# Optimization experiments

Hardware: AMD Instinct MI355X
Metric: run time of the kernel (lower is better)

The kernel has to match this reference:

```python
import jax, jax.numpy as jnp
import numpy as np

GRID_SIZE = 4
SPLINE_ORDER = 3
EDGE_DIM = 384


def make_grid():
    # efficient-KAN default grid_range [-1, 1]
    h = 2.0 / GRID_SIZE
    return (jnp.arange(-SPLINE_ORDER, GRID_SIZE + SPLINE_ORDER + 1, dtype=jnp.float32) * h - 1.0)


def b_splines(x, grid, k):
    # x: (N, d); grid: (G+2k+1,) shared across features -> (N, d, G+k)
    xe = x[..., None]
    bases = ((xe >= grid[:-1]) & (xe < grid[1:])).astype(x.dtype)
    for j in range(1, k + 1):
        bases = ((xe - grid[: -(j + 1)]) / (grid[j:-1] - grid[: -(j + 1)]) * bases[..., :-1]
                 + (grid[j + 1:] - xe) / (grid[j + 1:] - grid[1:-j]) * bases[..., 1:])
    return bases


def kan_linear(x, base_W, spline_W, grid):
    # efficient-KAN KANLinear: silu base path + spline path
    base = jax.nn.silu(x) @ base_W.T
    B = b_splines(x, grid, SPLINE_ORDER)          # (N, in, G+k)
    spline = jnp.einsum('nic,oic->no', B, spline_W)
    return base + spline


def gckan_layer(x, edge_index, edge_attr, p, grid):
    ea = edge_attr @ p['edge_W'].T + p['edge_b']          # (E, out)
    xt = x @ p['node_W'].T + p['node_b']                  # (N, out)
    row, col = edge_index[0], edge_index[1]
    msg = ea * xt[row]                                    # gather + multiply
    agg = jnp.zeros_like(xt).at[col].add(msg)             # scatter-add
    return kan_linear(agg, p['base_W'], p['spline_W'], grid)


def _layer_params(key, in_feat, out_feat):
    k1, k2, k3, k4 = jax.random.split(key, 4)
    coef = GRID_SIZE + SPLINE_ORDER
    return {
        'node_W': jax.random.normal(k1, (out_feat, in_feat), jnp.float32) / np.sqrt(in_feat),
        'node_b': jnp.zeros((out_feat,), jnp.float32),
        'edge_W': jax.random.normal(k2, (out_feat, EDGE_DIM), jnp.float32) / np.sqrt(EDGE_DIM),
        'edge_b': jnp.zeros((out_feat,), jnp.float32),
        'base_W': jax.random.normal(k3, (out_feat, out_feat), jnp.float32) / np.sqrt(out_feat),
        'spline_W': jax.random.normal(k4, (out_feat, out_feat, coef), jnp.float32) * (0.1 / np.sqrt(out_feat)),
    }


def setup_inputs() -> dict:
    N, E, F, H, C = 50000, 500000, 256, 256, 32
    key = jax.random.key(0)
    ks = jax.random.split(key, 6)
    inp = {
        'x': jax.random.normal(ks[0], (N, F), jnp.float32),
        'edge_index': jax.random.randint(ks[1], (2, E), 0, N, jnp.int32),
        'edge_attr': jax.random.normal(ks[2], (E, EDGE_DIM), jnp.float32),
    }
    p0 = _layer_params(ks[3], F, H)
    p1 = _layer_params(ks[4], H, H)
    po = _layer_params(ks[5], F + 2 * H, C)
    for tag, p in (('0', p0), ('1', p1), ('o', po)):
        for n, v in p.items():
            inp[n + tag] = v
    return inp


def reference(x, edge_index, edge_attr,
              node_W0, node_b0, edge_W0, edge_b0, base_W0, spline_W0,
              node_W1, node_b1, edge_W1, edge_b1, base_W1, spline_W1,
              node_Wo, node_bo, edge_Wo, edge_bo, base_Wo, spline_Wo):
    grid = make_grid()
    p0 = dict(node_W=node_W0, node_b=node_b0, edge_W=edge_W0, edge_b=edge_b0, base_W=base_W0, spline_W=spline_W0)
    p1 = dict(node_W=node_W1, node_b=node_b1, edge_W=edge_W1, edge_b=edge_b1, base_W=base_W1, spline_W=spline_W1)
    po = dict(node_W=node_Wo, node_b=node_bo, edge_W=edge_Wo, edge_b=edge_bo, base_W=base_Wo, spline_W=spline_Wo)
    skips = [x]
    h = gckan_layer(x, edge_index, edge_attr, p0, grid)
    skips.append(h)
    h = gckan_layer(h, edge_index, edge_attr, p1, grid)
    skips.append(h)
    h = jnp.concatenate(skips, axis=1)  # skip=True concat -> (N, F+2H)
    return gckan_layer(h, edge_index, edge_attr, po, grid)
```

## Files before the change

### kernel.cpp

```cpp
#include <hip/hip_runtime.h>


typedef __attribute__((ext_vector_type(4))) float f32x4;
typedef __attribute__((ext_vector_type(8))) short bf16x8;
typedef __attribute__((ext_vector_type(8))) unsigned short u16x8;
typedef __attribute__((ext_vector_type(4))) unsigned short u16x4;

__device__ __forceinline__ unsigned short f2bf(float f) {
    union { float f; unsigned u; } v; v.f = f;
    unsigned r = v.u + 0x7FFFu + ((v.u >> 16) & 1u);
    return (unsigned short)(r >> 16);
}

__device__ __forceinline__ float bf2f(unsigned short u) {
    union { unsigned u; float f; } v; v.u = ((unsigned)u) << 16;
    return v.f;
}

__device__ __forceinline__ float siluf(float x) {
    return x / (1.0f + __expf(-x));
}

__device__ __forceinline__ void gl16(const void* g, void* l) {
    __builtin_amdgcn_global_load_lds(
        (const __attribute__((address_space(1))) unsigned*)g,
        (__attribute__((address_space(3))) unsigned*)l, 16, 0, 0);
}

__device__ __forceinline__ void expand8(float x, float* o8) {
    float b[10];
#pragma unroll
    for (int i = 0; i < 10; ++i) {
        float ti = 0.5f * i - 2.5f;
        b[i] = (x >= ti && x < ti + 0.5f) ? 1.0f : 0.0f;
    }
#pragma unroll
    for (int j = 1; j <= 3; ++j) {
        float inv = 2.0f / (float)j;
#pragma unroll
        for (int i = 0; i < 10 - j; ++i) {
            float ti = 0.5f * i - 2.5f;
            float tj = 0.5f * (i + j + 1) - 2.5f;
            b[i] = (x - ti) * inv * b[i] + (tj - x) * inv * b[i + 1];
        }
    }
    o8[0] = siluf(x);
#pragma unroll
    for (int c = 0; c < 7; ++c) o8[c + 1] = b[c];
}

__global__ __launch_bounds__(256) void k_hist(
    const int* __restrict__ col, int* __restrict__ cnt, int E) {
    int i = blockIdx.x * 256 + threadIdx.x;
    if (i < E) atomicAdd(&cnt[col[i]], 1);
}

__global__ __launch_bounds__(1024) void k_scan(int* __restrict__ c, int N) {
    __shared__ int wsum[16];
    __shared__ int ctot;
    const int t = threadIdx.x;
    const int lane = t & 63, wid = t >> 6;
    int carry = 0;
    for (int base = 0; base < N; base += 1024) {
        int i = base + t;
        int v0 = (i < N) ? c[i] : 0;
        int v = v0;
#pragma unroll
        for (int off = 1; off < 64; off <<= 1) {
            int n = __shfl_up(v, (unsigned)off, 64);
            if (lane >= off) v += n;
        }
        if (lane == 63) wsum[wid] = v;
        __syncthreads();
        if (t < 16) {
            int s = wsum[t], sv = s;
#pragma unroll
            for (int off = 1; off < 16; off <<= 1) {
                int n = __shfl_up(sv, (unsigned)off, 16);
                if (t >= off) sv += n;
            }
            wsum[t] = sv - s;
            if (t == 15) ctot = sv;
        }
        __syncthreads();
        if (i < N) c[i] = carry + wsum[wid] + v - v0;
        carry += ctot;
        __syncthreads();
    }
}

__global__ __launch_bounds__(256) void k_scatter(
    const int* __restrict__ row, const int* __restrict__ col,
    int* __restrict__ cursor, int* __restrict__ rowS,
    int* __restrict__ colS, int* __restrict__ eidS, int E) {
    int i = blockIdx.x * 256 + threadIdx.x;
    if (i < E) {
        int c = col[i];
        int p = atomicAdd(&cursor[c], 1);
        rowS[p] = row[i];
        colS[p] = c;
        eidS[p] = i;
    }
}

__global__ __launch_bounds__(256) void pack_kt(
    const float* __restrict__ src, unsigned short* __restrict__ dst,
    int N, int K) {
    long idx = (long)blockIdx.x * 256 + threadIdx.x;
    if (idx >= (long)N * K) return;
    int n = (int)(idx / K), k = (int)(idx - (long)n * K);
    long o = (((long)(k >> 5) * 4 + ((k >> 3) & 3)) * N + n) * 8 + (k & 7);
    dst[o] = f2bf(src[idx]);
}

__global__ __launch_bounds__(256) void pack_kan_kt(
    const float* __restrict__ baseW, const float* __restrict__ splineW,
    unsigned short* __restrict__ dst, int N) {
    long idx = (long)blockIdx.x * 256 + threadIdx.x;
    if (idx >= (long)N * 2048) return;
    int n = (int)(idx >> 11), k = (int)(idx & 2047);
    int ic = k >> 3, c = k & 7;
    float v = (c == 0) ? baseW[(long)n * 256 + ic]
                       : splineW[((long)n * 256 + ic) * 7 + (c - 1)];
    long o = (((long)(k >> 5) * 4 + ((k >> 3) & 3)) * N + n) * 8 + (k & 7);
    dst[o] = f2bf(v);
}

template <bool TWO, bool WITH_O>
__global__ __launch_bounds__(256, 1) void ea_gemm6(
    const float* __restrict__ EA,
    const unsigned short* __restrict__ Wp0, const float* __restrict__ b0,
    const unsigned short* __restrict__ Wp1, const float* __restrict__ b1,
    const unsigned short* __restrict__ Wpo, const float* __restrict__ bo,
    unsigned short* __restrict__ O0, unsigned short* __restrict__ O1,
    unsigned short* __restrict__ Oo, int E) {
    constexpr int BSZ = TWO ? 32768 : 16384;
    constexpr int WOOFF = 8192 + 3 * BSZ;
    constexpr int SMEMSZ = WOOFF + (WITH_O ? 24576 : 0);
    __shared__ __align__(16) char smem[SMEMSZ];

    const int tid = threadIdx.x;
    const int wv = tid >> 6, lane = tid & 63;
    const int l15 = lane & 15, l4 = lane >> 4;
    const long m0 = (long)blockIdx.x * 64;

    f32x4 acc0[4][4] = {};
    f32x4 acc1[4][4] = {};
    f32x4 acco[4] = {};

    const int sr = tid >> 2, sg = tid & 3;
    const long arow = m0 + sr;
    const bool aok = arow < E;
    const float* aptr = EA + arow * 384 + sg * 8;
    const int awoff = sg * 1024 + ((sr ^ (sg << 2))) * 16;

    const char* wp0 = (const char*)Wp0;
    const char* wp1 = (const char*)Wp1;
    const int ci = lane * 16;

    if (WITH_O) {
#pragma unroll
        for (int i = 0; i < 6; ++i) {
            int o = (tid + i * 256) * 16;
            *(u16x8*)(smem + WOOFF + o) = *(const u16x8*)((const char*)Wpo + o);
        }
    }

#define ISSUE_B6(IT, BUF)                                                      \
    {                                                                          \
        _Pragma("unroll")                                                      \
        for (int g = 0; g < 4; ++g) {                                          \
            int ch = g * 4 + wv;                                               \
            gl16(wp0 + (long)(IT) * 16384 + ch * 1024 + ci,                    \
                 smem + 8192 + (BUF) * BSZ + ch * 1024);                       \
        }                                                                      \
        if (TWO) {                                                             \
            _Pragma("unroll")                                                  \
            for (int g = 0; g < 4; ++g) {                                      \
                int ch = g * 4 + wv;                                           \
                gl16(wp1 + (long)(IT) * 16384 + ch * 1024 + ci,                \
                     smem + 8192 + (BUF) * BSZ + 16384 + ch * 1024);           \
            }                                                                  \
        }                                                                      \
        __builtin_amdgcn_sched_barrier(0);                                     \
    }

#define WRITE_A6(IT, VA, VB)                                                   \
    {                                                                          \
        u16x8 rr = {};                                                         \
        if (aok) {                                                             \
            rr[0] = f2bf((VA).x); rr[1] = f2bf((VA).y);                        \
            rr[2] = f2bf((VA).z); rr[3] = f2bf((VA).w);                        \
            rr[4] = f2bf((VB).x); rr[5] = f2bf((VB).y);                        \
            rr[6] = f2bf((VB).z); rr[7] = f2bf((VB).w);                        \
        }                                                                      \
        *(u16x8*)(smem + ((IT) & 1) * 4096 + awoff) = rr;                      \
        __builtin_amdgcn_sched_barrier(0);                                     \
    }

    const float4 z4 = make_float4(0.f, 0.f, 0.f, 0.f);
    {
        float4 s0 = z4, s1 = z4;
        if (aok) { s0 = *(const float4*)(aptr); s1 = *(const float4*)(aptr + 4); }
        WRITE_A6(0, s0, s1);
    }
    float4 r1a = z4, r1b = z4, r0a = z4, r0b = z4;
    if (aok) { r1a = *(const float4*)(aptr + 32); r1b = *(const float4*)(aptr + 36); }
    __builtin_amdgcn_sched_barrier(0);
    ISSUE_B6(0, 0);
    if (aok) { r0a = *(const float4*)(aptr + 64); r0b = *(const float4*)(aptr + 68); }
    __builtin_amdgcn_sched_barrier(0);
    ISSUE_B6(1, 1);

#pragma unroll
    for (int it = 0; it < 12; ++it) {
        if (it <= 9) {
            if (TWO) asm volatile("s_waitcnt vmcnt(10)" ::: "memory");
            else     asm volatile("s_waitcnt vmcnt(6)"  ::: "memory");
        } else if (it == 10) {
            if (TWO) asm volatile("s_waitcnt vmcnt(8)" ::: "memory");
            else     asm volatile("s_waitcnt vmcnt(4)" ::: "memory");
        } else {
            asm volatile("s_waitcnt vmcnt(0)" ::: "memory");
        }
        asm volatile("s_waitcnt lgkmcnt(0)" ::: "memory");
        __builtin_amdgcn_s_barrier();
        __builtin_amdgcn_sched_barrier(0);

        if (it < 11) {
            if ((it + 1) & 1) { WRITE_A6(it + 1, r1a, r1b); }
            else              { WRITE_A6(it + 1, r0a, r0b); }
        }
        if (it <= 8) {
            if ((it + 3) & 1) {
                if (aok) {
                    r1a = *(const float4*)(aptr + (it + 3) * 32);
                    r1b = *(const float4*)(aptr + (it + 3) * 32 + 4);
                }
            } else {
                if (aok) {
                    r0a = *(const float4*)(aptr + (it + 3) * 32);
                    r0b = *(const float4*)(aptr + (it + 3) * 32 + 4);
                }
            }
            __builtin_amdgcn_sched_barrier(0);
        }
        if (it <= 9) { ISSUE_B6(it + 2, (it + 2) % 3); }

        const int abuf = it & 1, bbuf = it % 3;
        bf16x8 af[4];
#pragma unroll
        for (int mi = 0; mi < 4; ++mi)
            af[mi] = *(const bf16x8*)(smem + abuf * 4096 + l4 * 1024 +
                                      (((mi * 16 + l15) ^ (l4 << 2))) * 16);
        {
            bf16x8 bf0[4];
#pragma unroll
            for (int nj = 0; nj < 4; ++nj)
                bf0[nj] = *(const bf16x8*)(smem + 8192 + bbuf * BSZ + l4 * 4096 +
                                           (wv * 64 + nj * 16 + l15) * 16);
#pragma unroll
            for (int mi = 0; mi < 4; ++mi)
#pragma unroll
                for (int nj = 0; nj < 4; ++nj)
                    acc0[mi][nj] = __builtin_amdgcn_mfma_f32_16x16x32_bf16(
                        af[mi], bf0[nj], acc0[mi][nj], 0, 0, 0);
        }
        if (TWO) {
            bf16x8 bf1[4];
#pragma unroll
            for (int nj = 0; nj < 4; ++nj)
                bf1[nj] = *(const bf16x8*)(smem + 8192 + bbuf * BSZ + 16384 +
                                           l4 * 4096 + (wv * 64 + nj * 16 + l15) * 16);
#pragma unroll
            for (int mi = 0; mi < 4; ++mi)
#pragma unroll
                for (int nj = 0; nj < 4; ++nj)
                    acc1[mi][nj] = __builtin_amdgcn_mfma_f32_16x16x32_bf16(
                        af[mi], bf1[nj], acc1[mi][nj], 0, 0, 0);
        }
        if (WITH_O && wv < 2) {
            bf16x8 bov = *(const bf16x8*)(smem + WOOFF + it * 2048 + l4 * 512 +
                                          (wv * 16 + l15) * 16);
#pragma unroll
            for (int mi = 0; mi < 4; ++mi)
                acco[mi] = __builtin_amdgcn_mfma_f32_16x16x32_bf16(
                    af[mi], bov, acco[mi], 0, 0, 0);
        }
    }
#undef ISSUE_B6
#undef WRITE_A6

    const int nb2 = wv * 64;
    float bs0[4];
#pragma unroll
    for (int nj = 0; nj < 4; ++nj) bs0[nj] = b0[nb2 + nj * 16 + l15];
#pragma unroll
    for (int mi = 0; mi < 4; ++mi) {
#pragma unroll
        for (int r = 0; r < 4; ++r) {
            long e = m0 + mi * 16 + l4 * 4 + r;
            if (e < E) {
                unsigned short* dst = O0 + e * 256 + nb2 + l15;
#pragma unroll
                for (int nj = 0; nj < 4; ++nj)
                    dst[nj * 16] = f2bf(acc0[mi][nj][r] + bs0[nj]);
            }
        }
    }
    if (TWO) {
        float bs1[4];
#pragma unroll
        for (int nj = 0; nj < 4; ++nj) bs1[nj] = b1[nb2 + nj * 16 + l15];
#pragma unroll
        for (int mi = 0; mi < 4; ++mi) {
#pragma unroll
            for (int r = 0; r < 4; ++r) {
                long e = m0 + mi * 16 + l4 * 4 + r;
                if (e < E) {
                    unsigned short* dst = O1 + e * 256 + nb2 + l15;
#pragma unroll
                    for (int nj = 0; nj < 4; ++nj)
                        dst[nj * 16] = f2bf(acc1[mi][nj][r] + bs1[nj]);
                }
            }
        }
    }
    if (WITH_O && wv < 2) {
        float bso = bo[wv * 16 + l15];
#pragma unroll
        for (int mi = 0; mi < 4; ++mi) {
#pragma unroll
            for (int r = 0; r < 4; ++r) {
                long e = m0 + mi * 16 + l4 * 4 + r;
                if (e < E)
                    Oo[e * 32 + wv * 16 + l15] = f2bf(acco[mi][r] + bso);
            }
        }
    }
}

__global__ __launch_bounds__(256) void kan_mfma256_p(
    const float* __restrict__ AGG, const unsigned short* __restrict__ Wp,
    float* __restrict__ Y, int M) {
    __shared__ __align__(16) char smem[8192 + 2 * 16384];
    const int tid = threadIdx.x;
    const int wv = tid >> 6, lane = tid & 63;
    const int l15 = lane & 15, l4 = lane >> 4;
    const long m0 = (long)blockIdx.x * 64;
    f32x4 acc[4][4] = {};

    const int srow = tid & 63, sg = tid >> 6;
    const long arow = m0 + srow;
    const bool aok = arow < M;
    const float* aptr = AGG + arow * 256 + sg;
    const char* wp = (const char*)Wp;
    const int ci = lane * 16;
    const int awoff = sg * 1024 + srow * 16;

#define ISSUE_KB(IT, BUF)                                                      \
    {                                                                          \
        _Pragma("unroll")                                                      \
        for (int g = 0; g < 4; ++g) {                                          \
            int ch = g * 4 + wv;                                               \
            gl16(wp + (long)(IT) * 16384 + ch * 1024 + ci,                     \
                 smem + 8192 + (BUF) * 16384 + ch * 1024);                     \
        }                                                                      \
        __builtin_amdgcn_sched_barrier(0);                                     \
    }

    float xv0 = aok ? aptr[0] : 0.f;
    ISSUE_KB(0, 0);
    {
        float e8[8];
        expand8(xv0, e8);
        u16x8 ap;
#pragma unroll
        for (int c = 0; c < 8; ++c) ap[c] = f2bf(e8[c]);
        *(u16x8*)(smem + awoff) = ap;
    }
    float xv1 = aok ? aptr[4] : 0.f;
    __builtin_amdgcn_sched_barrier(0);

    for (int it = 0; it < 64; ++it) {
        if (it == 63) asm volatile("s_waitcnt vmcnt(0)" ::: "memory");
        else          asm volatile("s_waitcnt vmcnt(1)" ::: "memory");
        asm volatile("s_waitcnt lgkmcnt(0)" ::: "memory");
        __builtin_amdgcn_s_barrier();
        __builtin_amdgcn_sched_barrier(0);
        const int buf = it & 1, nbf = buf ^ 1;
        if (it < 63) {
            ISSUE_KB(it + 1, nbf);
            {
                float e8[8];
                expand8(xv1, e8);
                u16x8 ap;
#pragma unroll
                for (int c = 0; c < 8; ++c) ap[c] = f2bf(e8[c]);
                *(u16x8*)(smem + nbf * 4096 + awoff) = ap;
            }
            __builtin_amdgcn_sched_barrier(0);
            if (it < 62) {
                xv1 = aok ? aptr[(it + 2) * 4] : 0.f;
                __builtin_amdgcn_sched_barrier(0);
            }
        }
        bf16x8 af[4], bfv[4];
#pragma unroll
        for (int mi = 0; mi < 4; ++mi)
            af[mi] = *(const bf16x8*)(smem + buf * 4096 + l4 * 1024 +
                                      (mi * 16 + l15) * 16);
#pragma unroll
        for (int nj = 0; nj < 4; ++nj)
            bfv[nj] = *(const bf16x8*)(smem + 8192 + buf * 16384 + l4 * 4096 +
                                       (wv * 64 + nj * 16 + l15) * 16);
#pragma unroll
        for (int mi = 0; mi < 4; ++mi)
#pragma unroll
            for (int nj = 0; nj < 4; ++nj)
                acc[mi][nj] = __builtin_amdgcn_mfma_f32_16x16x32_bf16(
                    af[mi], bfv[nj], acc[mi][nj], 0, 0, 0);
    }
#undef ISSUE_KB

    const int nb = wv * 64;
#pragma unroll
    for (int mi = 0; mi < 4; ++mi) {
#pragma unroll
        for (int r = 0; r < 4; ++r) {
            long gm = m0 + mi * 16 + l4 * 4 + r;
            if (gm < M) {
#pragma unroll
                for (int nj = 0; nj < 4; ++nj)
                    Y[gm * 256 + nb + nj * 16 + l15] = acc[mi][nj][r];
            }
        }
    }
}

template <int K>
__global__ __launch_bounds__(256) void node_mfma_p(
    const float* __restrict__ X, const unsigned short* __restrict__ Wp,
    const float* __restrict__ bias, unsigned short* __restrict__ Y, int M) {
    __shared__ __align__(16) char smem[8192 + 2 * 16384];
    const int tid = threadIdx.x;
    const int wv = tid >> 6, lane = tid & 63;
    const int l15 = lane & 15, l4 = lane >> 4;
    const long m0 = (long)blockIdx.x * 64;
    f32x4 acc[4][4] = {};
    constexpr int NIT = K / 32;

    const int sr = tid >> 2, sg = tid & 3;
    const long arow = m0 + sr;
    const bool aok = arow < M;
    const float* aptr = X + arow * K + sg * 8;
    const int awoff = sg * 1024 + ((sr ^ (sg << 2))) * 16;
    const char* wp = (const char*)Wp;
    const int ci = lane * 16;

#define ISSUE_NB(IT, BUF)                                                      \
    {                                                                          \
        _Pragma("unroll")                                                      \
        for (int g = 0; g < 4; ++g) {                                          \
            int ch = g * 4 + wv;                                               \
            gl16(wp + (long)(IT) * 16384 + ch * 1024 + ci,                     \
                 smem + 8192 + (BUF) * 16384 + ch * 1024);                     \
        }                                                                      \
        __builtin_amdgcn_sched_barrier(0);                                     \
    }

#define WRITE_NA(BUF)                                                          \
    {                                                                          \
        u16x8 rr = {};                                                         \
        if (aok) {                                                             \
            rr[0] = f2bf(a0v.x); rr[1] = f2bf(a0v.y);                          \
            rr[2] = f2bf(a0v.z); rr[3] = f2bf(a0v.w);                          \
            rr[4] = f2bf(a1v.x); rr[5] = f2bf(a1v.y);                          \
            rr[6] = f2bf(a1v.z); rr[7] = f2bf(a1v.w);                          \
        }                                                                      \
        *(u16x8*)(smem + (BUF) * 4096 + awoff) = rr;                           \
        __builtin_amdgcn_sched_barrier(0);                                     \
    }

    ISSUE_NB(0, 0);
    float4 a0v = make_float4(0.f, 0.f, 0.f, 0.f);
    float4 a1v = make_float4(0.f, 0.f, 0.f, 0.f);
    if (aok) { a0v = *(const float4*)(aptr); a1v = *(const float4*)(aptr + 4); }
    WRITE_NA(0);
    if (aok) { a0v = *(const float4*)(aptr + 32); a1v = *(const float4*)(aptr + 36); }
    __builtin_amdgcn_sched_barrier(0);

#pragma unroll
    for (int it = 0; it < NIT; ++it) {
        if (it == NIT - 1) asm volatile("s_waitcnt vmcnt(0)" ::: "memory");
        else               asm volatile("s_waitcnt vmcnt(2)" ::: "memory");
        asm volatile("s_waitcnt lgkmcnt(0)" ::: "memory");
        __builtin_amdgcn_s_barrier();
        __builtin_amdgcn_sched_barrier(0);
        const int buf = it & 1, nbf = buf ^ 1;
        if (it < NIT - 1) {
            ISSUE_NB(it + 1, nbf);
            WRITE_NA(nbf);
            if (it < NIT - 2) {
                if (aok) {
                    a0v = *(const float4*)(aptr + (it + 2) * 32);
                    a1v = *(const float4*)(aptr + (it + 2) * 32 + 4);
                }
                __builtin_amdgcn_sched_barrier(0);
            }
        }
        bf16x8 af[4], bfv[4];
#pragma unroll
        for (int mi = 0; mi < 4; ++mi)
            af[mi] = *(const bf16x8*)(smem + buf * 4096 + l4 * 1024 +
                                      (((mi * 16 + l15) ^ (l4 << 2))) * 16);
#pragma unroll
        for (int nj = 0; nj < 4; ++nj)
            bfv[nj] = *(const bf16x8*)(smem + 8192 + buf * 16384 + l4 * 4096 +
                                       (wv * 64 + nj * 16 + l15) * 16);
#pragma unroll
        for (int mi = 0; mi < 4; ++mi)
#pragma unroll
            for (int nj = 0; nj < 4; ++nj)
                acc[mi][nj] = __builtin_amdgcn_mfma_f32_16x16x32_bf16(
                    af[mi], bfv[nj], acc[mi][nj], 0, 0, 0);
    }
#undef ISSUE_NB
#undef WRITE_NA

    const int nb = wv * 64;
    float bs[4];
#pragma unroll
    for (int nj = 0; nj < 4; ++nj) bs[nj] = bias[nb + nj * 16 + l15];
#pragma unroll
    for (int mi = 0; mi < 4; ++mi) {
#pragma unroll
        for (int r = 0; r < 4; ++r) {
            long gm = m0 + mi * 16 + l4 * 4 + r;
            if (gm < M) {
#pragma unroll
                for (int nj = 0; nj < 4; ++nj)
                    Y[gm * 256 + nb + nj * 16 + l15] = f2bf(acc[mi][nj][r] + bs[nj]);
            }
        }
    }
}

__global__ __launch_bounds__(256) void msg256(
    const unsigned short* __restrict__ EAr, const unsigned short* __restrict__ XT,
    const int* __restrict__ rowS, const int* __restrict__ colS,
    const int* __restrict__ eidS, float* __restrict__ AGG, int E) {
    __shared__ __align__(16) unsigned short eas[64][264];
    __shared__ int rows_s[64];
    __shared__ int cols_s[64];
    const int tid = threadIdx.x;
    const long m0 = (long)blockIdx.x * 64;

    const int r = tid >> 2, s = tid & 3;
    {
        long p = m0 + r;
        if (p < E) {
            const unsigned short* src = EAr + (long)eidS[p] * 256 + s * 8;
#pragma unroll
            for (int k = 0; k < 8; ++k)
                *(u16x8*)&eas[r][s * 8 + k * 32] = *(const u16x8*)(src + k * 32);
        } else {
            u16x8 z = {};
#pragma unroll
            for (int k = 0; k < 8; ++k) *(u16x8*)&eas[r][s * 8 + k * 32] = z;
        }
    }
    if (tid < 64) {
        long p = m0 + tid;
        cols_s[tid] = (p < E) ? colS[p] : -1;
        rows_s[tid] = (p < E) ? rowS[p] : 0;
    }
    __syncthreads();

    const int c = tid;
    float sum = 0.f;
    int cur = cols_s[0];
    int runstart = 0;
#pragma unroll 1
    for (int g = 0; g < 8; ++g) {
        float xv[8];
#pragma unroll
        for (int j = 0; j < 8; ++j)
            xv[j] = bf2f(XT[(long)rows_s[g * 8 + j] * 256 + c]);
#pragma unroll
        for (int j = 0; j < 8; ++j) {
            int e = g * 8 + j;
            int cc = cols_s[e];
            if (cc != cur) {
                if (cur >= 0) {
                    float* dst = AGG + (long)cur * 256 + c;
                    if (runstart > 0) *dst = sum;
                    else atomicAdd(dst, sum);
                }
                cur = cc; runstart = e; sum = 0.f;
            }
            sum += bf2f(eas[e][c]) * xv[j];
        }
    }
    if (cur >= 0) {
        atomicAdd(AGG + (long)cur * 256 + c, sum);
    }
}

__global__ __launch_bounds__(256) void msg32(
    const unsigned short* __restrict__ EAro, const unsigned short* __restrict__ XT,
    const int* __restrict__ rowS, const int* __restrict__ colS,
    const int* __restrict__ eidS, float* __restrict__ AGG, int E) {
    __shared__ __align__(16) unsigned short eas[256][36];
    __shared__ int rows_s[256];
    __shared__ int cols_s[256];
    __shared__ int eid_s[256];
    const int tid = threadIdx.x;
    const long m0 = (long)blockIdx.x * 256;

    {
        long p = m0 + tid;
        cols_s[tid] = (p < E) ? colS[p] : -1;
        rows_s[tid] = (p < E) ? rowS[p] : 0;
        eid_s[tid]  = (p < E) ? eidS[p] : -1;
    }
    __syncthreads();
    const int rr0 = tid >> 2, s = tid & 3;
#pragma unroll
    for (int ps = 0; ps < 4; ++ps) {
        int rr = ps * 64 + rr0;
        int eid = eid_s[rr];
        u16x8 v = {};
        if (eid >= 0) v = *(const u16x8*)(EAro + (long)eid * 32 + s * 8);
        *(u16x8*)&eas[rr][s * 8] = v;
    }
    __syncthreads();

    const int c = tid & 31, sb = tid >> 5;
    const int e0 = sb * 32;
    float sum = 0.f;
    int cur = cols_s[e0];
    int runstart = e0;
#pragma unroll 1
    for (int g = 0; g < 4; ++g) {
        float xv[8];
#pragma unroll
        for (int j = 0; j < 8; ++j)
            xv[j] = bf2f(XT[(long)rows_s[e0 + g * 8 + j] * 32 + c]);
#pragma unroll
        for (int j = 0; j < 8; ++j) {
            int e = e0 + g * 8 + j;
            int cc = cols_s[e];
            if (cc != cur) {
                if (cur >= 0) {
                    float* dst = AGG + (long)cur * 32 + c;
                    if (runstart > 0 && cols_s[runstart - 1] != cur) *dst = sum;
                    else atomicAdd(dst, sum);
                }
                cur = cc; runstart = e; sum = 0.f;
            }
            sum += bf2f(eas[e][c]) * xv[j];
        }
    }
    if (cur >= 0) {
        int eend = e0 + 32;
        float* dst = AGG + (long)cur * 32 + c;
        bool oks = (runstart > 0 && cols_s[runstart - 1] != cur);
        bool oke = (eend < 256 && cols_s[eend] != cur);
        if (oks && oke) *dst = sum;
        else atomicAdd(dst, sum);
    }
}

__global__ __launch_bounds__(256) void node_cat_mfma(
    const float* __restrict__ X, const float* __restrict__ H0,
    const float* __restrict__ H1, const unsigned short* __restrict__ Wh,
    const float* __restrict__ bias, unsigned short* __restrict__ Y, int M) {
    __shared__ __align__(16) unsigned short As[4][256][8];
    __shared__ __align__(16) unsigned short Bs[4][32][8];
    const int tid = threadIdx.x;
    const int wv = tid >> 6, lane = tid & 63;
    const int l15 = lane & 15, l4 = lane >> 4;
    const long m0 = (long)blockIdx.x * 256;
    f32x4 acc[4][2] = {};

    const int sr = tid >> 3;
    const int sq = (tid & 7) * 4;
    const int sg2 = sq >> 3, so2 = sq & 7;

    for (int it = 0; it < 24; ++it) {
        const int k0 = it * 32;
        const float* src = (it < 8) ? X : (it < 16) ? H0 : H1;
        const int kk = k0 & 255;
        float4 va[8];
#pragma unroll
        for (int j = 0; j < 8; ++j) {
            long r_ = m0 + j * 32 + sr;
            va[j] = (r_ < M) ? *(const float4*)(src + r_ * 256 + kk + sq)
                             : make_float4(0.f, 0.f, 0.f, 0.f);
        }
        u16x8 bv = {};
        if (tid < 128)
            bv = *(const u16x8*)(Wh + (long)(tid >> 2) * 768 + k0 + (tid & 3) * 8);
        __syncthreads();
#pragma unroll
        for (int j = 0; j < 8; ++j) {
            u16x4 ap;
            ap[0] = f2bf(va[j].x); ap[1] = f2bf(va[j].y);
            ap[2] = f2bf(va[j].z); ap[3] = f2bf(va[j].w);
            *(u16x4*)&As[sg2][j * 32 + sr][so2] = ap;
        }
        if (tid < 128) *(u16x8*)&Bs[tid & 3][tid >> 2][0] = bv;
        __syncthreads();
        bf16x8 af[4], bfv[2];
#pragma unroll
        for (int mi = 0; mi < 4; ++mi)
            af[mi] = *(const bf16x8*)&As[l4][wv * 64 + mi * 16 + l15][0];
#pragma unroll
        for (int nj = 0; nj < 2; ++nj)
            bfv[nj] = *(const bf16x8*)&Bs[l4][nj * 16 + l15][0];
#pragma unroll
        for (int mi = 0; mi < 4; ++mi)
#pragma unroll
            for (int nj = 0; nj < 2; ++nj)
                acc[mi][nj] = __builtin_amdgcn_mfma_f32_16x16x32_bf16(
                    af[mi], bfv[nj], acc[mi][nj], 0, 0, 0);
    }

#pragma unroll
    for (int mi = 0; mi < 4; ++mi) {
#pragma unroll
        for (int r = 0; r < 4; ++r) {
            long gm = m0 + wv * 64 + mi * 16 + l4 * 4 + r;
            if (gm < M) {
#pragma unroll
                for (int nj = 0; nj < 2; ++nj) {
                    int o = nj * 16 + l15;
                    Y[gm * 32 + o] = f2bf(acc[mi][nj][r] + bias[o]);
                }
            }
        }
    }
}

__global__ __launch_bounds__(256) void kan_gemm32(
    const float* __restrict__ AGG, const float* __restrict__ Wc,
    float* __restrict__ Y, int M) {
    __shared__ float As[64][36];
    __shared__ float Bs[32][36];
    const int tid = threadIdx.x;
    const int tx = tid & 15, ty = tid >> 4;
    const int m0 = blockIdx.x * 64;
    float acc[4][2] = {{0.f, 0.f}, {0.f, 0.f}, {0.f, 0.f}, {0.f, 0.f}};
    const int er = tid >> 2, ef = tid & 3;
    const int em = m0 + er;
    for (int ic = 0; ic < 32; ic += 4) {
        float xv = (em < M) ? AGG[(long)em * 32 + ic + ef] : 0.f;
        float e8[8];
        expand8(xv, e8);
        *(float4*)&As[er][ef * 8] = make_float4(e8[0], e8[1], e8[2], e8[3]);
        *(float4*)&As[er][ef * 8 + 4] = make_float4(e8[4], e8[5], e8[6], e8[7]);
        {
            int o = tid >> 3, k4 = (tid & 7) * 4;
            *(float4*)&Bs[o][k4] = *(const float4*)&Wc[(long)o * 256 + ic * 8 + k4];
        }
        __syncthreads();
#pragma unroll
        for (int kk = 0; kk < 32; ++kk) {
            float a_[4], b_[2];
#pragma unroll
            for (int i = 0; i < 4; ++i) a_[i] = As[ty * 4 + i][kk];
#pragma unroll
            for (int j = 0; j < 2; ++j) b_[j] = Bs[tx * 2 + j][kk];
#pragma unroll
            for (int i = 0; i < 4; ++i)
#pragma unroll
                for (int j = 0; j < 2; ++j) acc[i][j] = fmaf(a_[i], b_[j], acc[i][j]);
        }
        __syncthreads();
    }
#pragma unroll
    for (int i = 0; i < 4; ++i) {
        int gm = m0 + ty * 4 + i;
        if (gm >= M) continue;
#pragma unroll
        for (int j = 0; j < 2; ++j) Y[(long)gm * 32 + tx * 2 + j] = acc[i][j];
    }
}

__global__ __launch_bounds__(256) void cvt_bf16(
    const float* __restrict__ s, unsigned short* __restrict__ d, int n) {
    int i = blockIdx.x * 256 + threadIdx.x;
    if (i < n) d[i] = f2bf(s[i]);
}

__global__ __launch_bounds__(256) void pack_kan_f32(
    const float* __restrict__ baseW, const float* __restrict__ splineW,
    float* __restrict__ Wc, int n) {
    int idx = blockIdx.x * 256 + threadIdx.x;
    if (idx >= n) return;
    float* dst = Wc + (long)idx * 8;
    dst[0] = baseW[idx];
    const float* sw = splineW + (long)idx * 7;
#pragma unroll
    for (int c = 0; c < 7; ++c) dst[1 + c] = sw[c];
}

extern "C" void kernel_launch(void* const* d_in, const int* in_sizes, int n_in,
                              void* d_out, int out_size, void* d_ws, size_t ws_size,
                              hipStream_t stream) {
    const float* x          = (const float*)d_in[0];
    const int*   edge_index = (const int*)d_in[1];
    const float* edge_attr  = (const float*)d_in[2];
    const float* node_W0 = (const float*)d_in[3];
    const float* node_b0 = (const float*)d_in[4];
    const float* edge_W0 = (const float*)d_in[5];
    const float* edge_b0 = (const float*)d_in[6];
    const float* base_W0 = (const float*)d_in[7];
    const float* spline_W0 = (const float*)d_in[8];
    const float* node_W1 = (const float*)d_in[9];
    const float* node_b1 = (const float*)d_in[10];
    const float* edge_W1 = (const float*)d_in[11];
    const float* edge_b1 = (const float*)d_in[12];
    const float* base_W1 = (const float*)d_in[13];
    const float* spline_W1 = (const float*)d_in[14];
    const float* node_Wo = (const float*)d_in[15];
    const float* node_bo = (const float*)d_in[16];
    const float* edge_Wo = (const float*)d_in[17];
    const float* edge_bo = (const float*)d_in[18];
    const float* base_Wo = (const float*)d_in[19];
    const float* spline_Wo = (const float*)d_in[20];
    float* out = (float*)d_out;

    const int N = in_sizes[0] / 256;
    const int E = in_sizes[1] / 2;

    float* ws  = (float*)d_ws;
    unsigned short* xt = (unsigned short*)ws;
    float* agg = ws + (long)N * 256;
    float* h0  = agg + (long)N * 256;
    float* h1  = h0 + (long)N * 256;
    float* Wco = h1 + (long)N * 256;
    unsigned short* Wp0  = (unsigned short*)(Wco + 32 * 256);
    unsigned short* Wp1  = Wp0 + 98304;
    unsigned short* Wpo  = Wp1 + 98304;
    unsigned short* nWp0 = Wpo + 12288;
    unsigned short* nWp1 = nWp0 + 65536;
    unsigned short* Wc0p = nWp1 + 65536;
    unsigned short* Wc1p = Wc0p + 524288;
    unsigned short* nWoh = Wc1p + 524288;
    int* cursor = (int*)(nWoh + 24576);
    int* rowS   = cursor + (N + 1);
    int* colS   = rowS + E;
    int* eidS   = colS + E;
    unsigned short* EAr0 = (unsigned short*)(((uintptr_t)(eidS + E) + 255) & ~(uintptr_t)255);
    const int nt256 = (E + 255) / 256;
    const long Epad = (long)nt256 * 256;
    unsigned short* EAr1 = EAr0 + Epad * 256;

    const size_t need2 = (size_t)((char*)(EAr1 + Epad * 256 + Epad * 32) - (char*)d_ws);
    const bool two = ws_size >= need2;
    unsigned short* EAro = two ? (EAr1 + Epad * 256) : (EAr0 + Epad * 256);

    const int* row = edge_index;
    const int* col = edge_index + E;

    const int nb64 = (N + 63) / 64;
    const int eb64 = (E + 63) / 64;
    const int eb256 = (E + 255) / 256;
    const int nb256 = (N + 255) / 256;

    hipMemsetAsync(cursor, 0, (size_t)(N + 1) * sizeof(int), stream);
    k_hist<<<eb256, 256, 0, stream>>>(col, cursor, E);
    k_scan<<<1, 1024, 0, stream>>>(cursor, N);
    k_scatter<<<eb256, 256, 0, stream>>>(row, col, cursor, rowS, colS, eidS, E);

    pack_kt<<<(256 * 384 + 255) / 256, 256, 0, stream>>>(edge_W0, Wp0, 256, 384);
    pack_kt<<<(256 * 384 + 255) / 256, 256, 0, stream>>>(edge_W1, Wp1, 256, 384);
    pack_kt<<<(32 * 384 + 255) / 256, 256, 0, stream>>>(edge_Wo, Wpo, 32, 384);
    pack_kt<<<(256 * 256 + 255) / 256, 256, 0, stream>>>(node_W0, nWp0, 256, 256);
    pack_kt<<<(256 * 256 + 255) / 256, 256, 0, stream>>>(node_W1, nWp1, 256, 256);
    pack_kan_kt<<<(256 * 2048 + 255) / 256, 256, 0, stream>>>(base_W0, spline_W0, Wc0p, 256);
    pack_kan_kt<<<(256 * 2048 + 255) / 256, 256, 0, stream>>>(base_W1, spline_W1, Wc1p, 256);
    cvt_bf16<<<(32 * 768 + 255) / 256, 256, 0, stream>>>(node_Wo, nWoh, 32 * 768);
    pack_kan_f32<<<(32 * 32 + 255) / 256, 256, 0, stream>>>(base_Wo, spline_Wo, Wco, 32 * 32);

    if (two) {
        ea_gemm6<true, true><<<eb64, 256, 0, stream>>>(
            edge_attr, Wp0, edge_b0, Wp1, edge_b1, Wpo, edge_bo,
            EAr0, EAr1, EAro, E);
    } else {
        ea_gemm6<false, true><<<eb64, 256, 0, stream>>>(
            edge_attr, Wp0, edge_b0, Wp0, edge_b0, Wpo, edge_bo,
            EAr0, EAr0, EAro, E);
    }

    hipMemsetAsync(agg, 0, (size_t)N * 256 * sizeof(float), stream);
    node_mfma_p<256><<<nb64, 256, 0, stream>>>(x, nWp0, node_b0, xt, N);
    msg256<<<eb64, 256, 0, stream>>>(EAr0, xt, rowS, colS, eidS, agg, E);
    kan_mfma256_p<<<nb64, 256, 0, stream>>>(agg, Wc0p, h0, N);

    if (!two) {
        ea_gemm6<false, false><<<eb64, 256, 0, stream>>>(
            edge_attr, Wp1, edge_b1, Wp1, edge_b1, Wpo, edge_bo,
            EAr0, EAr0, EAro, E);
    }
    hipMemsetAsync(agg, 0, (size_t)N * 256 * sizeof(float), stream);
    node_mfma_p<256><<<nb64, 256, 0, stream>>>(h0, nWp1, node_b1, xt, N);
    msg256<<<eb64, 256, 0, stream>>>(two ? EAr1 : EAr0, xt, rowS, colS, eidS, agg, E);
    kan_mfma256_p<<<nb64, 256, 0, stream>>>(agg, Wc1p, h1, N);

    hipMemsetAsync(agg, 0, (size_t)N * 32 * sizeof(float), stream);
    node_cat_mfma<<<nb256, 256, 0, stream>>>(x, h0, h1, nWoh, node_bo, xt, N);
    msg32<<<eb256, 256, 0, stream>>>(EAro, xt, rowS, colS, eidS, agg, E);
    kan_gemm32<<<nb64, 256, 0, stream>>>(agg, Wco, out, N);
}
```

Baseline: 1.459 ms.

## Double-buffer edge GEMM weights and stream Wo tiles to fit two blocks per CU

The edge-attribute GEMM kernel goes from a triple-buffered B pipeline with a fully preloaded Wo slice to a double-buffered pipeline. The Wo weights now stream per K-step through global_load_lds, issued by the two waves that do not run the Wo MFMAs. The smaller LDS footprint plus launch_bounds(256,2) is meant to let two blocks share a CU and hide memory latency across blocks. In exchange, prefetch depth drops to one stage and the tighter vmcnt waits may stall more within a block, and the register cap may cause spills given the two 4x4 accumulator arrays.

```diff
diff --git a/kernel.cpp b/kernel.cpp
--- a/kernel.cpp
+++ b/kernel.cpp
@@ -127,7 +127,7 @@
 }
 
 template <bool TWO, bool WITH_O>
-__global__ __launch_bounds__(256, 1) void ea_gemm6(
+__global__ __launch_bounds__(256, 2) void ea_gemm7(
     const float* __restrict__ EA,
     const unsigned short* __restrict__ Wp0, const float* __restrict__ b0,
     const unsigned short* __restrict__ Wp1, const float* __restrict__ b1,
@@ -135,8 +135,8 @@
     unsigned short* __restrict__ O0, unsigned short* __restrict__ O1,
     unsigned short* __restrict__ Oo, int E) {
     constexpr int BSZ = TWO ? 32768 : 16384;
-    constexpr int WOOFF = 8192 + 3 * BSZ;
-    constexpr int SMEMSZ = WOOFF + (WITH_O ? 24576 : 0);
+    constexpr int WOOFF = 8192 + 2 * BSZ;
+    constexpr int SMEMSZ = WOOFF + (WITH_O ? 4096 : 0);
     __shared__ __align__(16) char smem[SMEMSZ];
 
     const int tid = threadIdx.x;
@@ -156,17 +156,10 @@
 
     const char* wp0 = (const char*)Wp0;
     const char* wp1 = (const char*)Wp1;
+    const char* wpo = (const char*)Wpo;
     const int ci = lane * 16;
 
-    if (WITH_O) {
-#pragma unroll
-        for (int i = 0; i < 6; ++i) {
-            int o = (tid + i * 256) * 16;
-            *(u16x8*)(smem + WOOFF + o) = *(const u16x8*)((const char*)Wpo + o);
-        }
-    }
-
-#define ISSUE_B6(IT, BUF)                                                      \
+#define ISSUE_B7(IT, BUF)                                                      \
     {                                                                          \
         _Pragma("unroll")                                                      \
         for (int g = 0; g < 4; ++g) {                                          \
@@ -185,7 +178,15 @@
         __builtin_amdgcn_sched_barrier(0);                                     \
     }
 
-#define WRITE_A6(IT, VA, VB)                                                   \
+#define ISSUE_WO7(IT, BUF)                                                     \
+    {                                                                          \
+        if (WITH_O && wv >= 2)                                                 \
+            gl16(wpo + (long)(IT) * 2048 + (wv - 2) * 1024 + ci,               \
+                 smem + WOOFF + (BUF) * 2048 + (wv - 2) * 1024);               \
+        __builtin_amdgcn_sched_barrier(0);                                     \
+    }
+
+#define WRITE_A7(IT, VA, VB)                                                   \
     {                                                                          \
         u16x8 rr = {};                                                         \
         if (aok) {                                                             \
@@ -202,62 +203,57 @@
     {
         float4 s0 = z4, s1 = z4;
         if (aok) { s0 = *(const float4*)(aptr); s1 = *(const float4*)(aptr + 4); }
-        WRITE_A6(0, s0, s1);
+        WRITE_A7(0, s0, s1);
     }
     float4 r1a = z4, r1b = z4, r0a = z4, r0b = z4;
     if (aok) { r1a = *(const float4*)(aptr + 32); r1b = *(const float4*)(aptr + 36); }
     __builtin_amdgcn_sched_barrier(0);
-    ISSUE_B6(0, 0);
+    ISSUE_B7(0, 0);
+    ISSUE_WO7(0, 0);
     if (aok) { r0a = *(const float4*)(aptr + 64); r0b = *(const float4*)(aptr + 68); }
     __builtin_amdgcn_sched_barrier(0);
-    ISSUE_B6(1, 1);
 
 #pragma unroll
     for (int it = 0; it < 12; ++it) {
-        if (it <= 9) {
-            if (TWO) asm volatile("s_waitcnt vmcnt(10)" ::: "memory");
-            else     asm volatile("s_waitcnt vmcnt(6)"  ::: "memory");
-        } else if (it == 10) {
-            if (TWO) asm volatile("s_waitcnt vmcnt(8)" ::: "memory");
-            else     asm volatile("s_waitcnt vmcnt(4)" ::: "memory");
-        } else {
-            asm volatile("s_waitcnt vmcnt(0)" ::: "memory");
-        }
+        if (it <= 9) asm volatile("s_waitcnt vmcnt(2)" ::: "memory");
+        else         asm volatile("s_waitcnt vmcnt(0)" ::: "memory");
         asm volatile("s_waitcnt lgkmcnt(0)" ::: "memory");
         __builtin_amdgcn_s_barrier();
         __builtin_amdgcn_sched_barrier(0);
 
         if (it < 11) {
-            if ((it + 1) & 1) { WRITE_A6(it + 1, r1a, r1b); }
-            else              { WRITE_A6(it + 1, r0a, r0b); }
-        }
-        if (it <= 8) {
-            if ((it + 3) & 1) {
-                if (aok) {
-                    r1a = *(const float4*)(aptr + (it + 3) * 32);
-                    r1b = *(const float4*)(aptr + (it + 3) * 32 + 4);
+            const int nbf = (it + 1) & 1;
+            ISSUE_B7(it + 1, nbf);
+            ISSUE_WO7(it + 1, nbf);
+            if ((it + 1) & 1) { WRITE_A7(it + 1, r1a, r1b); }
+            else              { WRITE_A7(it + 1, r0a, r0b); }
+            if (it <= 8) {
+                if ((it + 3) & 1) {
+                    if (aok) {
+                        r1a = *(const float4*)(aptr + (it + 3) * 32);
+                        r1b = *(const float4*)(aptr + (it + 3) * 32 + 4);
+                    }
+                } else {
+                    if (aok) {
+                        r0a = *(const float4*)(aptr + (it + 3) * 32);
+                        r0b = *(const float4*)(aptr + (it + 3) * 32 + 4);
+                    }
                 }
-            } else {
-                if (aok) {
-                    r0a = *(const float4*)(aptr + (it + 3) * 32);
-                    r0b = *(const float4*)(aptr + (it + 3) * 32 + 4);
-                }
-            }
-            __builtin_amdgcn_sched_barrier(0);
-        }
-        if (it <= 9) { ISSUE_B6(it + 2, (it + 2) % 3); }
-
-        const int abuf = it & 1, bbuf = it % 3;
+                __builtin_amdgcn_sched_barrier(0);
+            }
+        }
+
+        const int buf = it & 1;
         bf16x8 af[4];
 #pragma unroll
         for (int mi = 0; mi < 4; ++mi)
-            af[mi] = *(const bf16x8*)(smem + abuf * 4096 + l4 * 1024 +
+            af[mi] = *(const bf16x8*)(smem + buf * 4096 + l4 * 1024 +
                                       (((mi * 16 + l15) ^ (l4 << 2))) * 16);
         {
             bf16x8 bf0[4];
 #pragma unroll
             for (int nj = 0; nj < 4; ++nj)
-                bf0[nj] = *(const bf16x8*)(smem + 8192 + bbuf * BSZ + l4 * 4096 +
+                bf0[nj] = *(const bf16x8*)(smem + 8192 + buf * BSZ + l4 * 4096 +
                                            (wv * 64 + nj * 16 + l15) * 16);
 #pragma unroll
             for (int mi = 0; mi < 4; ++mi)
@@ -270,7 +266,7 @@
             bf16x8 bf1[4];
 #pragma unroll
             for (int nj = 0; nj < 4; ++nj)
-                bf1[nj] = *(const bf16x8*)(smem + 8192 + bbuf * BSZ + 16384 +
+                bf1[nj] = *(const bf16x8*)(smem + 8192 + buf * BSZ + 16384 +
                                            l4 * 4096 + (wv * 64 + nj * 16 + l15) * 16);
 #pragma unroll
             for (int mi = 0; mi < 4; ++mi)
@@ -280,7 +276,7 @@
                         af[mi], bf1[nj], acc1[mi][nj], 0, 0, 0);
         }
         if (WITH_O && wv < 2) {
-            bf16x8 bov = *(const bf16x8*)(smem + WOOFF + it * 2048 + l4 * 512 +
+            bf16x8 bov = *(const bf16x8*)(smem + WOOFF + buf * 2048 + l4 * 512 +
                                           (wv * 16 + l15) * 16);
 #pragma unroll
             for (int mi = 0; mi < 4; ++mi)
@@ -288,8 +284,9 @@
                     af[mi], bov, acco[mi], 0, 0, 0);
         }
     }
-#undef ISSUE_B6
-#undef WRITE_A6
+#undef ISSUE_B7
+#undef ISSUE_WO7
+#undef WRITE_A7
 
     const int nb2 = wv * 64;
     float bs0[4];
@@ -886,11 +883,11 @@
     pack_kan_f32<<<(32 * 32 + 255) / 256, 256, 0, stream>>>(base_Wo, spline_Wo, Wco, 32 * 32);
 
     if (two) {
-        ea_gemm6<true, true><<<eb64, 256, 0, stream>>>(
+        ea_gemm7<true, true><<<eb64, 256, 0, stream>>>(
             edge_attr, Wp0, edge_b0, Wp1, edge_b1, Wpo, edge_bo,
             EAr0, EAr1, EAro, E);
     } else {
-        ea_gemm6<false, true><<<eb64, 256, 0, stream>>>(
+        ea_gemm7<false, true><<<eb64, 256, 0, stream>>>(
             edge_attr, Wp0, edge_b0, Wp0, edge_b0, Wpo, edge_bo,
             EAr0, EAr0, EAro, E);
     }
@@ -901,7 +898,7 @@
     kan_mfma256_p<<<nb64, 256, 0, stream>>>(agg, Wc0p, h0, N);
 
     if (!two) {
-        ea_gemm6<false, false><<<eb64, 256, 0, stream>>>(
+        ea_gemm7<false, false><<<eb64, 256, 0, stream>>>(
             edge_attr, Wp1, edge_b1, Wp1, edge_b1, Wpo, edge_bo,
             EAr0, EAr0, EAro, E);
     }
```

Result: faster. 1.319 ms (median of 2 runs) (-9.6%).
